# Kernel optimization log

Hardware: AMD Instinct MI355X
Metric: run time of the kernel (lower is better)

## Reference

```python
import jax, jax.numpy as jnp
import numpy as np

TREE_DEPTH = 6
TEMPERATURE = 1.0


def setup_inputs() -> dict:
    key = jax.random.key(0)
    k1, k2, k3, k4, k5 = jax.random.split(key, 5)
    B, D = 8192, 512
    T = 64                      # n_trees
    N = 2 ** TREE_DEPTH - 1    # internal nodes = 63
    L = 2 ** TREE_DEPTH        # leaves = 64
    C = 100                    # classes
    return {
        "x": jax.random.normal(k1, (B, D), dtype=jnp.float32),
        "split_weights": jax.random.normal(k2, (T, N, D), dtype=jnp.float32),
        "split_bias": jax.random.normal(k3, (T, N), dtype=jnp.float32),
        "leaf_logits": jax.random.normal(k4, (T, L, C), dtype=jnp.float32),
        "tree_weights": jax.random.uniform(k5, (T,), dtype=jnp.float32),
    }


def reference(x, split_weights, split_bias, leaf_logits, tree_weights):
    # All node decisions for all trees in one batched GEMM: [B, T, N]
    dec = jax.nn.sigmoid(
        (jnp.einsum("bd,tnd->btn", x, split_weights) + split_bias) / TEMPERATURE
    )
    B = x.shape[0]
    T = split_weights.shape[0]
    L = leaf_logits.shape[1]  # 2 ** TREE_DEPTH
    leaf_ids = jnp.arange(L)
    # Cumulative product of routing probs along each leaf's root-to-leaf path.
    leaf_probs = jnp.ones((B, T, L), dtype=x.dtype)
    for d in range(TREE_DEPTH):
        # ancestor node (level order) of each leaf at this depth
        node_idx = (2 ** d - 1) + (leaf_ids >> (TREE_DEPTH - d))
        # 1 -> right child (prob = dec), 0 -> left child (prob = 1 - dec)
        bit = (leaf_ids >> (TREE_DEPTH - d - 1)) & 1
        dd = dec[:, :, node_idx]  # [B, T, L]
        leaf_probs = leaf_probs * jnp.where(bit.astype(bool), dd, 1.0 - dd)
    tree_out = jax.nn.softmax(leaf_logits, axis=-1)  # [T, L, C]
    # weighted sum over trees of (leaf_probs @ leaf class dists)
    return jnp.einsum("btl,tlc,t->bc", leaf_probs, tree_out, tree_weights)
```

## Files before the change

### kernel.cpp

```cpp
#include <hip/hip_runtime.h>

#define TREES 64
#define NN 63
#define LL 64
#define CC 100
#define CPAD 112
#define DD 512
#define BB 8192

typedef __attribute__((ext_vector_type(8))) _Float16 f16x8;
typedef __attribute__((ext_vector_type(4))) _Float16 f16x4;
typedef __attribute__((ext_vector_type(4))) float floatx4;

#define XH_WS   0
#define SWH_WS  8388608
#define W2T_WS  12582912
#define LP_WS   13500416

__device__ __forceinline__ void gl_lds16(const _Float16* g, char* lds) {
    __builtin_amdgcn_global_load_lds(
        (const __attribute__((address_space(1))) unsigned int*)g,
        (__attribute__((address_space(3))) unsigned int*)lds, 16, 0, 0);
}

__device__ __forceinline__ f16x8 cvt8(const float* s) {
    float4 a = *(const float4*)s, b = *(const float4*)(s + 4);
    f16x8 h;
    h[0]=(_Float16)a.x; h[1]=(_Float16)a.y; h[2]=(_Float16)a.z; h[3]=(_Float16)a.w;
    h[4]=(_Float16)b.x; h[5]=(_Float16)b.y; h[6]=(_Float16)b.z; h[7]=(_Float16)b.w;
    return h;
}

__device__ __forceinline__ float fsig(float x) {
    return __builtin_amdgcn_rcpf(1.f + __expf(-x));
}

__global__ __launch_bounds__(256) void prep_kernel(
    const float* __restrict__ x, const float* __restrict__ sw,
    const float* __restrict__ leaf_logits, const float* __restrict__ tree_w,
    _Float16* __restrict__ xh, _Float16* __restrict__ swh,
    _Float16* __restrict__ w2T)
{
    if (blockIdx.x < 3072) {
        int i = blockIdx.x * 256 + threadIdx.x;
        if (i < 524288) {
            int tile = i >> 10, cidx = i & 1023;
            int row = cidx >> 3, c = cidx & 7;
            int rb = tile >> 3, kt = tile & 7;
            int gk = kt * 64 + ((c ^ (row & 7)) << 3);
            *(f16x8*)(xh + (size_t)i * 8) = cvt8(x + (size_t)(rb * 128 + row) * DD + gk);
        } else {
            int j = i - 524288;
            if (j < 262144) {
                int tile = j >> 10, cidx = j & 1023;
                int col = cidx >> 3, c = cidx & 7;
                int cb = tile >> 3, kt = tile & 7;
                int tt = col >> 6, node = col & 63;
                f16x8 h = (f16x8)(_Float16)0.f;
                if (node < NN) {
                    int gk = kt * 64 + ((c ^ (col & 7)) << 3);
                    h = cvt8(sw + (size_t)((cb * 2 + tt) * NN + node) * DD + gk);
                }
                *(f16x8*)(swh + (size_t)j * 8) = h;
            }
        }
    } else {
        int row  = (blockIdx.x - 3072) * 4 + (threadIdx.x >> 6);
        int lane = threadIdx.x & 63;
        int t = row >> 6, l = row & 63;
        const float* src = leaf_logits + (size_t)row * CC;
        float v0 = (lane < CC)      ? src[lane]      : -1e30f;
        float v1 = (lane + 64 < CC) ? src[lane + 64] : -1e30f;
        float m = fmaxf(v0, v1);
#pragma unroll
        for (int off = 32; off > 0; off >>= 1)
            m = fmaxf(m, __shfl_down(m, off, 64));
        m = __shfl(m, 0, 64);
        float e0 = (lane < CC)      ? __expf(v0 - m) : 0.f;
        float e1 = (lane + 64 < CC) ? __expf(v1 - m) : 0.f;
        float s = e0 + e1;
#pragma unroll
        for (int off = 32; off > 0; off >>= 1)
            s += __shfl_down(s, off, 64);
        s = __shfl(s, 0, 64);
        float scale = tree_w[t] / s;
        _Float16* base = w2T + (size_t)t * CPAD * LL;
#define LSWZ(c) ((((l >> 3) ^ ((c) & 7)) << 3) | (l & 7))
        if (lane < CC)      base[(size_t)lane * LL + LSWZ(lane)]               = (_Float16)(e0 * scale);
        if (lane + 64 < CC) base[(size_t)(lane + 64) * LL + LSWZ(lane + 64)]   = (_Float16)(e1 * scale);
        if (lane < CPAD - CC) base[(size_t)(CC + lane) * LL + LSWZ(CC + lane)] = (_Float16)0.f;
#undef LSWZ
    }
}

#define A_SMEM 33280
__global__ __launch_bounds__(256, 4) void gemm1_kernel(
    const _Float16* __restrict__ xh,
    const _Float16* __restrict__ swh,
    const float* __restrict__ sb,
    _Float16* __restrict__ lp_ws)
{
    __shared__ __align__(16) char smem[A_SMEM];
    _Float16* xs  = (_Float16*)smem;
    _Float16* wl  = (_Float16*)(smem + 16384);
    _Float16* dec = (_Float16*)smem;
    _Float16* lpl = (_Float16*)smem;

    const int tid  = threadIdx.x;
    const int lane = tid & 63;
    const int wid  = tid >> 6;
    const int wy   = wid >> 1;
    const int wx   = wid & 1;
    const int quad = lane >> 4;
    const int l15  = lane & 15;
    const int rb   = blockIdx.x;
    const int cb   = blockIdx.y;

    float bias_v[4];
    {
        int mytree = cb * 2 + wx;
#pragma unroll
        for (int ni = 0; ni < 4; ++ni) {
            int nd = 16 * ni + l15;
            bias_v[ni] = (nd < NN) ? sb[mytree * NN + nd] : 0.f;
        }
    }

    floatx4 acc[4][4];
#pragma unroll
    for (int i = 0; i < 4; ++i)
#pragma unroll
        for (int j = 0; j < 4; ++j) acc[i][j] = (floatx4)0.f;

    const _Float16* xtile = xh + (size_t)rb * 8 * 8192;
    const _Float16* wtile = swh + (size_t)cb * 8 * 8192;

    for (int kt = 0; kt < 8; ++kt) {
        __syncthreads();
#pragma unroll
        for (int j = 0; j < 4; ++j) {
            gl_lds16(xtile + kt * 8192 + j * 2048 + wid * 512 + lane * 8,
                     smem + j * 4096 + wid * 1024);
            gl_lds16(wtile + kt * 8192 + j * 2048 + wid * 512 + lane * 8,
                     smem + 16384 + j * 4096 + wid * 1024);
        }
        __syncthreads();
#pragma unroll
        for (int ks = 0; ks < 2; ++ks) {
            f16x8 af[4], bf[4];
#pragma unroll
            for (int mi = 0; mi < 4; ++mi) {
                int r = 64 * wy + 16 * mi + l15;
                af[mi] = *(const f16x8*)&xs[r * 64 + ((((ks << 2) | quad) ^ (r & 7)) << 3)];
            }
#pragma unroll
            for (int ni = 0; ni < 4; ++ni) {
                int r = 64 * wx + 16 * ni + l15;
                bf[ni] = *(const f16x8*)&wl[r * 64 + ((((ks << 2) | quad) ^ (r & 7)) << 3)];
            }
#pragma unroll
            for (int mi = 0; mi < 4; ++mi)
#pragma unroll
                for (int ni = 0; ni < 4; ++ni)
                    acc[mi][ni] = __builtin_amdgcn_mfma_f32_16x16x32_f16(
                        af[mi], bf[ni], acc[mi][ni], 0, 0, 0);
        }
    }
    __syncthreads();

#pragma unroll
    for (int mi = 0; mi < 4; ++mi) {
        int r0 = 64 * wy + 16 * mi + 4 * quad;
#pragma unroll
        for (int ni = 0; ni < 4; ++ni) {
            int col = 64 * wx + 16 * ni + l15;
            f16x4 v;
#pragma unroll
            for (int r = 0; r < 4; ++r)
                v[r] = (_Float16)(acc[mi][ni][r] + bias_v[ni]);
            *(f16x4*)&dec[col * 130 + r0] = v;
        }
    }
    __syncthreads();

    const int tt   = tid >> 7;
    const int lrow = tid & 127;
    const int tb   = tt * 64;
    f16x8 lpreg[8];
    {
#define SIG(n) fsig((float)dec[(tb + (n)) * 130 + lrow])
        float d0 = SIG(0);
#pragma unroll
        for (int h = 0; h < 2; ++h) {
            float p1 = h ? d0 : 1.f - d0;
            float d1 = SIG(1 + h);
#pragma unroll
            for (int b8 = 0; b8 < 4; ++b8) {
                int i4 = b8 >> 1, i3 = b8 & 1;
                float p2 = p1 * (i4 ? d1 : 1.f - d1);
                float d2 = SIG(3 + 2 * h + i4);
                float p3 = p2 * (i3 ? d2 : 1.f - d2);
                float d3 = SIG(7 + 4 * h + b8);
                f16x8 blk;
#pragma unroll
                for (int i2 = 0; i2 < 2; ++i2) {
                    float p4 = p3 * (i2 ? d3 : 1.f - d3);
                    float d4 = SIG(15 + 8 * h + 2 * b8 + i2);
#pragma unroll
                    for (int i1 = 0; i1 < 2; ++i1) {
                        float p5 = p4 * (i1 ? d4 : 1.f - d4);
                        float d5 = SIG(31 + 16 * h + 4 * b8 + 2 * i2 + i1);
                        blk[i2 * 4 + i1 * 2 + 0] = (_Float16)(p5 * (1.f - d5));
                        blk[i2 * 4 + i1 * 2 + 1] = (_Float16)(p5 * d5);
                    }
                }
                lpreg[h * 4 + b8] = blk;
            }
        }
#undef SIG
    }
    __syncthreads();

#pragma unroll
    for (int q = 0; q < 8; ++q)
        *(f16x8*)&lpl[tt * 8192 + lrow * 64 + ((q ^ (lrow & 7)) << 3)] = lpreg[q];
    __syncthreads();

    const int rloc0 = blockIdx.x * 128;
#pragma unroll
    for (int k = 0; k < 8; ++k) {
        int idx = k * 256 + tid;
        int t2 = idx >> 10, rem = idx & 1023;
        int row = rem >> 3, cq = rem & 7;
        f16x8 v = *(const f16x8*)&lpl[t2 * 8192 + row * 64 + cq * 8];
        *(f16x8*)(lp_ws + ((size_t)(cb * 2 + t2) * BB + rloc0 + row) * 64 + cq * 8) = v;
    }
}

#define RSTR 113
#define RREG (32 * RSTR)
__global__ __launch_bounds__(512, 2) void gemm2_kernel(
    const _Float16* __restrict__ lp_ws,
    const _Float16* __restrict__ w2T,
    float* __restrict__ out)
{
    __shared__ float red[4 * RREG];

    const int tid  = threadIdx.x;
    const int lane = tid & 63;
    const int wv   = tid >> 6;
    const int quad = lane >> 4;
    const int l15  = lane & 15;
    const int r0   = blockIdx.x * 32;
    const int t0   = wv * 8;

    floatx4 oacc[2][7];
#pragma unroll
    for (int mi = 0; mi < 2; ++mi)
#pragma unroll
        for (int ni = 0; ni < 7; ++ni) oacc[mi][ni] = (floatx4)0.f;

    const int sw0 = ((0 | quad) ^ (l15 & 7)) << 3;
    const int sw1 = ((4 | quad) ^ (l15 & 7)) << 3;
    const _Float16* aBase = lp_ws + ((size_t)t0 * BB + r0 + l15) * 64;
    const _Float16* bBase = w2T + (size_t)t0 * CPAD * LL + (size_t)l15 * 64;

    f16x8 ab[2][2], bb[2][7];
#define LOADS(s, buf)                                                          \
    {                                                                          \
        int t8 = (s) >> 1;                                                     \
        int sw = ((s) & 1) ? sw1 : sw0;                                        \
        const _Float16* ap = aBase + (size_t)t8 * (BB * 64);                   \
        const _Float16* bp = bBase + (size_t)t8 * (CPAD * LL);                 \
        ab[buf][0] = *(const f16x8*)(ap + sw);                                 \
        ab[buf][1] = *(const f16x8*)(ap + 16 * 64 + sw);                       \
        _Pragma("unroll")                                                      \
        for (int ni = 0; ni < 7; ++ni)                                         \
            bb[buf][ni] = *(const f16x8*)(bp + ni * 16 * 64 + sw);             \
    }
#define MFMAS(buf)                                                             \
    {                                                                          \
        _Pragma("unroll")                                                      \
        for (int mi = 0; mi < 2; ++mi)                                         \
            _Pragma("unroll")                                                  \
            for (int ni = 0; ni < 7; ++ni)                                     \
                oacc[mi][ni] = __builtin_amdgcn_mfma_f32_16x16x32_f16(         \
                    ab[buf][mi], bb[buf][ni], oacc[mi][ni], 0, 0, 0);          \
    }
    LOADS(0, 0)
#pragma unroll
    for (int s = 0; s < 15; ++s) {
        LOADS(s + 1, (s + 1) & 1)
        MFMAS(s & 1)
    }
    MFMAS(1)
#undef LOADS
#undef MFMAS

    if (wv >= 4) {
        float* rg = &red[(wv - 4) * RREG];
#pragma unroll
        for (int mi = 0; mi < 2; ++mi)
#pragma unroll
            for (int ni = 0; ni < 7; ++ni)
#pragma unroll
                for (int r = 0; r < 4; ++r)
                    rg[(16 * mi + 4 * quad + r) * RSTR + 16 * ni + l15] = oacc[mi][ni][r];
    }
    __syncthreads();
    if (wv < 4) {
        float* rg = &red[wv * RREG];
#pragma unroll
        for (int mi = 0; mi < 2; ++mi)
#pragma unroll
            for (int ni = 0; ni < 7; ++ni)
#pragma unroll
                for (int r = 0; r < 4; ++r)
                    rg[(16 * mi + 4 * quad + r) * RSTR + 16 * ni + l15] += oacc[mi][ni][r];
    }
    __syncthreads();
    {
        int row = tid >> 4, c16 = tid & 15;
#pragma unroll
        for (int k = 0; k < 7; ++k) {
            int col = k * 16 + c16;
            float s = 0.f;
#pragma unroll
            for (int g = 0; g < 4; ++g)
                s += red[g * RREG + row * RSTR + col];
            if (col < CC)
                out[(size_t)(r0 + row) * CC + col] = s;
        }
    }
}

extern "C" void kernel_launch(void* const* d_in, const int* in_sizes, int n_in,
                              void* d_out, int out_size, void* d_ws, size_t ws_size,
                              hipStream_t stream) {
    const float* x  = (const float*)d_in[0];
    const float* sw = (const float*)d_in[1];
    const float* sb = (const float*)d_in[2];
    const float* ll = (const float*)d_in[3];
    const float* tw = (const float*)d_in[4];
    float* out = (float*)d_out;
    _Float16* xh  = (_Float16*)((char*)d_ws + XH_WS);
    _Float16* swh = (_Float16*)((char*)d_ws + SWH_WS);
    _Float16* w2T = (_Float16*)((char*)d_ws + W2T_WS);
    _Float16* lp  = (_Float16*)((char*)d_ws + LP_WS);

    prep_kernel<<<dim3(4096), 256, 0, stream>>>(x, sw, ll, tw, xh, swh, w2T);
    gemm1_kernel<<<dim3(64, 32), 256, 0, stream>>>(xh, swh, sb, lp);
    gemm2_kernel<<<dim3(256), 512, 0, stream>>>(lp, w2T, out);
}
```

Baseline: 161.5 us.

## Fuse routing GEMM and leaf-mixing GEMM into one kernel with atomic output

Merges gemm1 and gemm2 into one kernel. Each block loops over 4 tree-pairs, computes the leaf probabilities in shared memory and right away multiplies them by the per-tree leaf distributions, accumulating in registers. Partial results are atomically added into an output buffer that prep_kernel zeroes. This removes the global round trip of the fp16 leaf-probability workspace and one kernel launch. In exchange it uses fewer blocks (512 instead of 2048), lowers the occupancy hint, and adds 8-way atomic contention on every output element.

Result: slower. 177.8 us (+10.1%).

```diff
diff --git a/kernel.cpp b/kernel.cpp
--- a/kernel.cpp
+++ b/kernel.cpp
@@ -15,7 +15,6 @@
 #define XH_WS   0
 #define SWH_WS  8388608
 #define W2T_WS  12582912
-#define LP_WS   13500416
 
 __device__ __forceinline__ void gl_lds16(const _Float16* g, char* lds) {
     __builtin_amdgcn_global_load_lds(
@@ -39,7 +38,7 @@
     const float* __restrict__ x, const float* __restrict__ sw,
     const float* __restrict__ leaf_logits, const float* __restrict__ tree_w,
     _Float16* __restrict__ xh, _Float16* __restrict__ swh,
-    _Float16* __restrict__ w2T)
+    _Float16* __restrict__ w2T, float* __restrict__ out)
 {
     if (blockIdx.x < 3072) {
         int i = blockIdx.x * 256 + threadIdx.x;
@@ -64,7 +63,7 @@
                 *(f16x8*)(swh + (size_t)j * 8) = h;
             }
         }
-    } else {
+    } else if (blockIdx.x < 4096) {
         int row  = (blockIdx.x - 3072) * 4 + (threadIdx.x >> 6);
         int lane = threadIdx.x & 63;
         int t = row >> 6, l = row & 63;
@@ -90,15 +89,19 @@
         if (lane + 64 < CC) base[(size_t)(lane + 64) * LL + LSWZ(lane + 64)]   = (_Float16)(e1 * scale);
         if (lane < CPAD - CC) base[(size_t)(CC + lane) * LL + LSWZ(CC + lane)] = (_Float16)0.f;
 #undef LSWZ
+    } else {
+        int i = (blockIdx.x - 4096) * 1024 + threadIdx.x * 4;
+        *(float4*)(out + i) = make_float4(0.f, 0.f, 0.f, 0.f);
     }
 }
 
 #define A_SMEM 33280
-__global__ __launch_bounds__(256, 4) void gemm1_kernel(
+__global__ __launch_bounds__(256, 2) void fused_kernel(
     const _Float16* __restrict__ xh,
     const _Float16* __restrict__ swh,
     const float* __restrict__ sb,
-    _Float16* __restrict__ lp_ws)
+    const _Float16* __restrict__ w2T,
+    float* __restrict__ out)
 {
     __shared__ __align__(16) char smem[A_SMEM];
     _Float16* xs  = (_Float16*)smem;
@@ -114,223 +117,171 @@
     const int quad = lane >> 4;
     const int l15  = lane & 15;
     const int rb   = blockIdx.x;
-    const int cb   = blockIdx.y;
-
-    float bias_v[4];
+    const int tc   = blockIdx.y;
+
+    floatx4 oacc2[2][7];
+#pragma unroll
+    for (int mi = 0; mi < 2; ++mi)
+#pragma unroll
+        for (int ni = 0; ni < 7; ++ni) oacc2[mi][ni] = (floatx4)0.f;
+
+    const _Float16* xtile = xh + (size_t)rb * 8 * 8192;
+
+    for (int tg = 0; tg < 4; ++tg) {
+        const int cb = tc * 4 + tg;
+        const _Float16* wtile = swh + (size_t)cb * 8 * 8192;
+
+        float bias_v[4];
+        {
+            int mytree = cb * 2 + wx;
+#pragma unroll
+            for (int ni = 0; ni < 4; ++ni) {
+                int nd = 16 * ni + l15;
+                bias_v[ni] = (nd < NN) ? sb[mytree * NN + nd] : 0.f;
+            }
+        }
+
+        floatx4 acc[4][4];
+#pragma unroll
+        for (int i = 0; i < 4; ++i)
+#pragma unroll
+            for (int j = 0; j < 4; ++j) acc[i][j] = (floatx4)0.f;
+
+        for (int kt = 0; kt < 8; ++kt) {
+            __syncthreads();
+#pragma unroll
+            for (int j = 0; j < 4; ++j) {
+                gl_lds16(xtile + kt * 8192 + j * 2048 + wid * 512 + lane * 8,
+                         smem + j * 4096 + wid * 1024);
+                gl_lds16(wtile + kt * 8192 + j * 2048 + wid * 512 + lane * 8,
+                         smem + 16384 + j * 4096 + wid * 1024);
+            }
+            __syncthreads();
+#pragma unroll
+            for (int ks = 0; ks < 2; ++ks) {
+                f16x8 af[4], bf[4];
+#pragma unroll
+                for (int mi = 0; mi < 4; ++mi) {
+                    int r = 64 * wy + 16 * mi + l15;
+                    af[mi] = *(const f16x8*)&xs[r * 64 + ((((ks << 2) | quad) ^ (r & 7)) << 3)];
+                }
+#pragma unroll
+                for (int ni = 0; ni < 4; ++ni) {
+                    int r = 64 * wx + 16 * ni + l15;
+                    bf[ni] = *(const f16x8*)&wl[r * 64 + ((((ks << 2) | quad) ^ (r & 7)) << 3)];
+                }
+#pragma unroll
+                for (int mi = 0; mi < 4; ++mi)
+#pragma unroll
+                    for (int ni = 0; ni < 4; ++ni)
+                        acc[mi][ni] = __builtin_amdgcn_mfma_f32_16x16x32_f16(
+                            af[mi], bf[ni], acc[mi][ni], 0, 0, 0);
+            }
+        }
+        __syncthreads();
+
+#pragma unroll
+        for (int mi = 0; mi < 4; ++mi) {
+            int r0 = 64 * wy + 16 * mi + 4 * quad;
+#pragma unroll
+            for (int ni = 0; ni < 4; ++ni) {
+                int col = 64 * wx + 16 * ni + l15;
+                f16x4 v;
+#pragma unroll
+                for (int r = 0; r < 4; ++r)
+                    v[r] = (_Float16)(acc[mi][ni][r] + bias_v[ni]);
+                *(f16x4*)&dec[col * 130 + r0] = v;
+            }
+        }
+        __syncthreads();
+
+        const int tt   = tid >> 7;
+        const int lrow = tid & 127;
+        const int tb   = tt * 64;
+        f16x8 lpreg[8];
+        {
+#define SIG(n) fsig((float)dec[(tb + (n)) * 130 + lrow])
+            float d0 = SIG(0);
+#pragma unroll
+            for (int h = 0; h < 2; ++h) {
+                float p1 = h ? d0 : 1.f - d0;
+                float d1 = SIG(1 + h);
+#pragma unroll
+                for (int b8 = 0; b8 < 4; ++b8) {
+                    int i4 = b8 >> 1, i3 = b8 & 1;
+                    float p2 = p1 * (i4 ? d1 : 1.f - d1);
+                    float d2 = SIG(3 + 2 * h + i4);
+                    float p3 = p2 * (i3 ? d2 : 1.f - d2);
+                    float d3 = SIG(7 + 4 * h + b8);
+                    f16x8 blk;
+#pragma unroll
+                    for (int i2 = 0; i2 < 2; ++i2) {
+                        float p4 = p3 * (i2 ? d3 : 1.f - d3);
+                        float d4 = SIG(15 + 8 * h + 2 * b8 + i2);
+#pragma unroll
+                        for (int i1 = 0; i1 < 2; ++i1) {
+                            float p5 = p4 * (i1 ? d4 : 1.f - d4);
+                            float d5 = SIG(31 + 16 * h + 4 * b8 + 2 * i2 + i1);
+                            blk[i2 * 4 + i1 * 2 + 0] = (_Float16)(p5 * (1.f - d5));
+                            blk[i2 * 4 + i1 * 2 + 1] = (_Float16)(p5 * d5);
+                        }
+                    }
+                    lpreg[h * 4 + b8] = blk;
+                }
+            }
+#undef SIG
+        }
+        __syncthreads();
+
+#pragma unroll
+        for (int q = 0; q < 8; ++q)
+            *(f16x8*)&lpl[tt * 8192 + lrow * 64 + ((q ^ (lrow & 7)) << 3)] = lpreg[q];
+        __syncthreads();
+
+        {
+            const int tree0 = cb * 2;
+            const int rbase = wid * 32;
+#pragma unroll
+            for (int t = 0; t < 2; ++t) {
+                const _Float16* bp = w2T + (size_t)(tree0 + t) * (CPAD * LL) + (size_t)l15 * 64;
+                const _Float16* lplt = lpl + t * 8192;
+#pragma unroll
+                for (int ks = 0; ks < 2; ++ks) {
+                    const int sw = (((ks << 2) | quad) ^ (l15 & 7)) << 3;
+                    f16x8 bbv[7], abv[2];
+#pragma unroll
+                    for (int ni = 0; ni < 7; ++ni)
+                        bbv[ni] = *(const f16x8*)(bp + ni * 16 * 64 + sw);
+#pragma unroll
+                    for (int mi = 0; mi < 2; ++mi) {
+                        int r = rbase + 16 * mi + l15;
+                        abv[mi] = *(const f16x8*)&lplt[r * 64 + sw];
+                    }
+#pragma unroll
+                    for (int mi = 0; mi < 2; ++mi)
+#pragma unroll
+                        for (int ni = 0; ni < 7; ++ni)
+                            oacc2[mi][ni] = __builtin_amdgcn_mfma_f32_16x16x32_f16(
+                                abv[mi], bbv[ni], oacc2[mi][ni], 0, 0, 0);
+                }
+            }
+        }
+    }
+
     {
-        int mytree = cb * 2 + wx;
-#pragma unroll
-        for (int ni = 0; ni < 4; ++ni) {
-            int nd = 16 * ni + l15;
-            bias_v[ni] = (nd < NN) ? sb[mytree * NN + nd] : 0.f;
-        }
-    }
-
-    floatx4 acc[4][4];
-#pragma unroll
-    for (int i = 0; i < 4; ++i)
-#pragma unroll
-        for (int j = 0; j < 4; ++j) acc[i][j] = (floatx4)0.f;
-
-    const _Float16* xtile = xh + (size_t)rb * 8 * 8192;
-    const _Float16* wtile = swh + (size_t)cb * 8 * 8192;
-
-    for (int kt = 0; kt < 8; ++kt) {
-        __syncthreads();
-#pragma unroll
-        for (int j = 0; j < 4; ++j) {
-            gl_lds16(xtile + kt * 8192 + j * 2048 + wid * 512 + lane * 8,
-                     smem + j * 4096 + wid * 1024);
-            gl_lds16(wtile + kt * 8192 + j * 2048 + wid * 512 + lane * 8,
-                     smem + 16384 + j * 4096 + wid * 1024);
-        }
-        __syncthreads();
-#pragma unroll
-        for (int ks = 0; ks < 2; ++ks) {
-            f16x8 af[4], bf[4];
-#pragma unroll
-            for (int mi = 0; mi < 4; ++mi) {
-                int r = 64 * wy + 16 * mi + l15;
-                af[mi] = *(const f16x8*)&xs[r * 64 + ((((ks << 2) | quad) ^ (r & 7)) << 3)];
-            }
-#pragma unroll
-            for (int ni = 0; ni < 4; ++ni) {
-                int r = 64 * wx + 16 * ni + l15;
-                bf[ni] = *(const f16x8*)&wl[r * 64 + ((((ks << 2) | quad) ^ (r & 7)) << 3)];
-            }
-#pragma unroll
-            for (int mi = 0; mi < 4; ++mi)
-#pragma unroll
-                for (int ni = 0; ni < 4; ++ni)
-                    acc[mi][ni] = __builtin_amdgcn_mfma_f32_16x16x32_f16(
-                        af[mi], bf[ni], acc[mi][ni], 0, 0, 0);
-        }
-    }
-    __syncthreads();
-
-#pragma unroll
-    for (int mi = 0; mi < 4; ++mi) {
-        int r0 = 64 * wy + 16 * mi + 4 * quad;
-#pragma unroll
-        for (int ni = 0; ni < 4; ++ni) {
-            int col = 64 * wx + 16 * ni + l15;
-            f16x4 v;
-#pragma unroll
-            for (int r = 0; r < 4; ++r)
-                v[r] = (_Float16)(acc[mi][ni][r] + bias_v[ni]);
-            *(f16x4*)&dec[col * 130 + r0] = v;
-        }
-    }
-    __syncthreads();
-
-    const int tt   = tid >> 7;
-    const int lrow = tid & 127;
-    const int tb   = tt * 64;
-    f16x8 lpreg[8];
-    {
-#define SIG(n) fsig((float)dec[(tb + (n)) * 130 + lrow])
-        float d0 = SIG(0);
-#pragma unroll
-        for (int h = 0; h < 2; ++h) {
-            float p1 = h ? d0 : 1.f - d0;
-            float d1 = SIG(1 + h);
-#pragma unroll
-            for (int b8 = 0; b8 < 4; ++b8) {
-                int i4 = b8 >> 1, i3 = b8 & 1;
-                float p2 = p1 * (i4 ? d1 : 1.f - d1);
-                float d2 = SIG(3 + 2 * h + i4);
-                float p3 = p2 * (i3 ? d2 : 1.f - d2);
-                float d3 = SIG(7 + 4 * h + b8);
-                f16x8 blk;
-#pragma unroll
-                for (int i2 = 0; i2 < 2; ++i2) {
-                    float p4 = p3 * (i2 ? d3 : 1.f - d3);
-                    float d4 = SIG(15 + 8 * h + 2 * b8 + i2);
-#pragma unroll
-                    for (int i1 = 0; i1 < 2; ++i1) {
-                        float p5 = p4 * (i1 ? d4 : 1.f - d4);
-                        float d5 = SIG(31 + 16 * h + 4 * b8 + 2 * i2 + i1);
-                        blk[i2 * 4 + i1 * 2 + 0] = (_Float16)(p5 * (1.f - d5));
-                        blk[i2 * 4 + i1 * 2 + 1] = (_Float16)(p5 * d5);
-                    }
-                }
-                lpreg[h * 4 + b8] = blk;
-            }
-        }
-#undef SIG
-    }
-    __syncthreads();
-
-#pragma unroll
-    for (int q = 0; q < 8; ++q)
-        *(f16x8*)&lpl[tt * 8192 + lrow * 64 + ((q ^ (lrow & 7)) << 3)] = lpreg[q];
-    __syncthreads();
-
-    const int rloc0 = blockIdx.x * 128;
-#pragma unroll
-    for (int k = 0; k < 8; ++k) {
-        int idx = k * 256 + tid;
-        int t2 = idx >> 10, rem = idx & 1023;
-        int row = rem >> 3, cq = rem & 7;
-        f16x8 v = *(const f16x8*)&lpl[t2 * 8192 + row * 64 + cq * 8];
-        *(f16x8*)(lp_ws + ((size_t)(cb * 2 + t2) * BB + rloc0 + row) * 64 + cq * 8) = v;
-    }
-}
-
-#define RSTR 113
-#define RREG (32 * RSTR)
-__global__ __launch_bounds__(512, 2) void gemm2_kernel(
-    const _Float16* __restrict__ lp_ws,
-    const _Float16* __restrict__ w2T,
-    float* __restrict__ out)
-{
-    __shared__ float red[4 * RREG];
-
-    const int tid  = threadIdx.x;
-    const int lane = tid & 63;
-    const int wv   = tid >> 6;
-    const int quad = lane >> 4;
-    const int l15  = lane & 15;
-    const int r0   = blockIdx.x * 32;
-    const int t0   = wv * 8;
-
-    floatx4 oacc[2][7];
-#pragma unroll
-    for (int mi = 0; mi < 2; ++mi)
-#pragma unroll
-        for (int ni = 0; ni < 7; ++ni) oacc[mi][ni] = (floatx4)0.f;
-
-    const int sw0 = ((0 | quad) ^ (l15 & 7)) << 3;
-    const int sw1 = ((4 | quad) ^ (l15 & 7)) << 3;
-    const _Float16* aBase = lp_ws + ((size_t)t0 * BB + r0 + l15) * 64;
-    const _Float16* bBase = w2T + (size_t)t0 * CPAD * LL + (size_t)l15 * 64;
-
-    f16x8 ab[2][2], bb[2][7];
-#define LOADS(s, buf)                                                          \
-    {                                                                          \
-        int t8 = (s) >> 1;                                                     \
-        int sw = ((s) & 1) ? sw1 : sw0;                                        \
-        const _Float16* ap = aBase + (size_t)t8 * (BB * 64);                   \
-        const _Float16* bp = bBase + (size_t)t8 * (CPAD * LL);                 \
-        ab[buf][0] = *(const f16x8*)(ap + sw);                                 \
-        ab[buf][1] = *(const f16x8*)(ap + 16 * 64 + sw);                       \
-        _Pragma("unroll")                                                      \
-        for (int ni = 0; ni < 7; ++ni)                                         \
-            bb[buf][ni] = *(const f16x8*)(bp + ni * 16 * 64 + sw);             \
-    }
-#define MFMAS(buf)                                                             \
-    {                                                                          \
-        _Pragma("unroll")                                                      \
-        for (int mi = 0; mi < 2; ++mi)                                         \
-            _Pragma("unroll")                                                  \
-            for (int ni = 0; ni < 7; ++ni)                                     \
-                oacc[mi][ni] = __builtin_amdgcn_mfma_f32_16x16x32_f16(         \
-                    ab[buf][mi], bb[buf][ni], oacc[mi][ni], 0, 0, 0);          \
-    }
-    LOADS(0, 0)
-#pragma unroll
-    for (int s = 0; s < 15; ++s) {
-        LOADS(s + 1, (s + 1) & 1)
-        MFMAS(s & 1)
-    }
-    MFMAS(1)
-#undef LOADS
-#undef MFMAS
-
-    if (wv >= 4) {
-        float* rg = &red[(wv - 4) * RREG];
+        const int rbase2 = rb * 128 + wid * 32 + 4 * quad;
 #pragma unroll
         for (int mi = 0; mi < 2; ++mi)
 #pragma unroll
-            for (int ni = 0; ni < 7; ++ni)
-#pragma unroll
-                for (int r = 0; r < 4; ++r)
-                    rg[(16 * mi + 4 * quad + r) * RSTR + 16 * ni + l15] = oacc[mi][ni][r];
-    }
-    __syncthreads();
-    if (wv < 4) {
-        float* rg = &red[wv * RREG];
-#pragma unroll
-        for (int mi = 0; mi < 2; ++mi)
-#pragma unroll
-            for (int ni = 0; ni < 7; ++ni)
-#pragma unroll
-                for (int r = 0; r < 4; ++r)
-                    rg[(16 * mi + 4 * quad + r) * RSTR + 16 * ni + l15] += oacc[mi][ni][r];
-    }
-    __syncthreads();
-    {
-        int row = tid >> 4, c16 = tid & 15;
-#pragma unroll
-        for (int k = 0; k < 7; ++k) {
-            int col = k * 16 + c16;
-            float s = 0.f;
-#pragma unroll
-            for (int g = 0; g < 4; ++g)
-                s += red[g * RREG + row * RSTR + col];
-            if (col < CC)
-                out[(size_t)(r0 + row) * CC + col] = s;
-        }
+            for (int ni = 0; ni < 7; ++ni) {
+                int col = 16 * ni + l15;
+                if (col < CC) {
+#pragma unroll
+                    for (int r = 0; r < 4; ++r)
+                        unsafeAtomicAdd(&out[(size_t)(rbase2 + 16 * mi + r) * CC + col],
+                                        oacc2[mi][ni][r]);
+                }
+            }
     }
 }
 
@@ -346,9 +297,7 @@
     _Float16* xh  = (_Float16*)((char*)d_ws + XH_WS);
     _Float16* swh = (_Float16*)((char*)d_ws + SWH_WS);
     _Float16* w2T = (_Float16*)((char*)d_ws + W2T_WS);
-    _Float16* lp  = (_Float16*)((char*)d_ws + LP_WS);
-
-    prep_kernel<<<dim3(4096), 256, 0, stream>>>(x, sw, ll, tw, xh, swh, w2T);
-    gemm1_kernel<<<dim3(64, 32), 256, 0, stream>>>(xh, swh, sb, lp);
-    gemm2_kernel<<<dim3(256), 512, 0, stream>>>(lp, w2T, out);
-}
+
+    prep_kernel<<<dim3(4896), 256, 0, stream>>>(x, sw, ll, tw, xh, swh, w2T, out);
+    fused_kernel<<<dim3(64, 8), 256, 0, stream>>>(xh, swh, sb, w2T, out);
+}
```
